# Kernel tuning notes

Measured on AMD Instinct MI355X. Metric: run time of the kernel, lower is better.

## Reference

```python
import jax, jax.numpy as jnp
import numpy as np

N_NODES = 50000
N_EDGES = 800000
IN_DIM = 6
HID = 256
OUT = 256
N_EXPERTS = 8
N_LAYERS = 2
N_GRAPHS = 64


def setup_inputs() -> dict:
    key = jax.random.key(0)
    ks = jax.random.split(key, 16)
    s = 0.05
    x = jax.random.normal(ks[0], (N_NODES, IN_DIM), dtype=jnp.float32)
    edge_index = jax.random.randint(ks[1], (2, N_EDGES), 0, N_NODES, dtype=jnp.int64)
    batch = jnp.sort(jax.random.randint(ks[2], (N_NODES,), 0, N_GRAPHS, dtype=jnp.int64))
    # shared encoder
    W_enc = jax.random.normal(ks[3], (IN_DIM, HID), jnp.float32) * s
    b_enc = jnp.zeros((HID,), jnp.float32)
    # router MLP: (HID+2) -> HID -> N_EXPERTS
    Wr1 = jax.random.normal(ks[4], (HID + 2, HID), jnp.float32) * s
    br1 = jnp.zeros((HID,), jnp.float32)
    Wr2 = jax.random.normal(ks[5], (HID, N_EXPERTS), jnp.float32) * s
    br2 = jnp.zeros((N_EXPERTS,), jnp.float32)
    # experts: 2 GraphConv layers each (self weight + neighbor weight + bias), stacked over experts
    Ws0 = jax.random.normal(ks[6], (N_EXPERTS, HID, HID), jnp.float32) * s
    Wn0 = jax.random.normal(ks[7], (N_EXPERTS, HID, HID), jnp.float32) * s
    b0 = jnp.zeros((N_EXPERTS, HID), jnp.float32)
    Ws1 = jax.random.normal(ks[8], (N_EXPERTS, HID, OUT), jnp.float32) * s
    Wn1 = jax.random.normal(ks[9], (N_EXPERTS, HID, OUT), jnp.float32) * s
    b1 = jnp.zeros((N_EXPERTS, OUT), jnp.float32)
    return dict(x=x, edge_index=edge_index, batch=batch, W_enc=W_enc, b_enc=b_enc,
                Wr1=Wr1, br1=br1, Wr2=Wr2, br2=br2,
                Ws0=Ws0, Wn0=Wn0, b0=b0, Ws1=Ws1, Wn1=Wn1, b1=b1)


def _graph_conv(h, src, dst, Ws, Wn, b):
    # PyG GraphConv: x' = x @ Ws + sum_{j in N(i)} x_j @ Wn + b
    msg = h[src] @ Wn                                   # [E, d_out]
    agg = jax.ops.segment_sum(msg, dst, num_segments=N_NODES)
    return h @ Ws + agg + b


def reference(x, edge_index, batch, W_enc, b_enc, Wr1, br1, Wr2, br2,
              Ws0, Wn0, b0, Ws1, Wn1, b1):
    src, dst = edge_index[0], edge_index[1]
    # shared encoder
    h = jax.nn.relu(x @ W_enc + b_enc)                  # [N, HID]
    # graph size features: per-graph node count and edge count, log-scaled, broadcast to nodes
    ones_n = jnp.ones((h.shape[0],), h.dtype)
    node_cnt = jax.ops.segment_sum(ones_n, batch, num_segments=N_GRAPHS)
    edge_cnt = jax.ops.segment_sum(jnp.ones((src.shape[0],), h.dtype), batch[src], num_segments=N_GRAPHS)
    size_feat = jnp.stack([jnp.log1p(node_cnt)[batch], jnp.log1p(edge_cnt)[batch]], axis=-1)  # [N, 2]
    # router -> top-1 expert index
    r = jax.nn.relu(jnp.concatenate([h, size_feat], axis=-1) @ Wr1 + br1)
    logits = r @ Wr2 + br2                              # [N, n_experts]
    idx = jnp.argmax(logits, axis=-1)                   # [N]
    # dense compute-all-experts, then gather by argmax (faithful to original)
    out = jnp.zeros((h.shape[0], Ws1.shape[-1]), h.dtype)
    for e in range(N_EXPERTS):
        z = jax.nn.relu(_graph_conv(h, src, dst, Ws0[e], Wn0[e], b0[e]))
        y_e = _graph_conv(z, src, dst, Ws1[e], Wn1[e], b1[e])   # [N, OUT]
        out = out + jnp.where((idx == e)[:, None], y_e, 0.0)
    return out
```

## Files before the change

kernel.cpp:

```cpp
#include <hip/hip_runtime.h>
#include <hip/hip_bf16.h>
#include <math.h>

#define NN 50000
#define NE 800000
#define NG 64
#define NEXP 8

#define BK 16
#define BM 64

typedef __attribute__((ext_vector_type(8))) short bf16x8;
typedef __attribute__((ext_vector_type(4))) float f32x4;
typedef unsigned short ushort_t;

__device__ __forceinline__ unsigned short f2bf(float f) {
  union { float f; unsigned u; } x; x.f = f;
  unsigned r = x.u + 0x7fff + ((x.u >> 16) & 1);
  return (unsigned short)(r >> 16);
}
__device__ __forceinline__ float bf2f(unsigned short u) {
  union { unsigned u; float f; } x; x.u = ((unsigned)u) << 16; return x.f;
}

__device__ __forceinline__ void gld16(const void* g, void* l) {
  __builtin_amdgcn_global_load_lds(
      (const __attribute__((address_space(1))) unsigned int*)g,
      (__attribute__((address_space(3))) unsigned int*)l, 16, 0, 0);
}

__global__ __launch_bounds__(256) void k_encoder(
    const float* __restrict__ x, const float* __restrict__ W,
    const float* __restrict__ b, float* __restrict__ H32,
    ushort_t* __restrict__ Xb, ushort_t* __restrict__ Xlo) {
  int i = blockIdx.x, n = threadIdx.x;
  float acc = b[n];
#pragma unroll
  for (int k = 0; k < 6; k++) acc = fmaf(x[i * 6 + k], W[k * 256 + n], acc);
  acc = fmaxf(acc, 0.f);
  H32[i * 256 + n] = acc;
  unsigned short hb = f2bf(acc);
  Xb[(size_t)i * 512 + n] = hb;
  Xlo[(size_t)i * 256 + n] = f2bf(acc - bf2f(hb));
}

__global__ __launch_bounds__(256) void k_count_nodes(
    const int* __restrict__ batch, int* __restrict__ node_cnt) {
  __shared__ int bins[NG];
  int t = threadIdx.x;
  if (t < NG) bins[t] = 0;
  __syncthreads();
  for (int i = blockIdx.x * blockDim.x + t; i < NN; i += gridDim.x * blockDim.x)
    atomicAdd(&bins[batch[i]], 1);
  __syncthreads();
  if (t < NG) atomicAdd(&node_cnt[t], bins[t]);
}

__global__ __launch_bounds__(256) void k_count_edges(
    const int* __restrict__ ei, const int* __restrict__ batch,
    int* __restrict__ edge_cnt, int* __restrict__ deg) {
  __shared__ int bins[NG];
  int t = threadIdx.x;
  if (t < NG) bins[t] = 0;
  __syncthreads();
  for (int e = blockIdx.x * blockDim.x + t; e < NE; e += gridDim.x * blockDim.x) {
    int s = ei[e];
    int d = ei[NE + e];
    atomicAdd(&bins[batch[s]], 1);
    atomicAdd(&deg[d], 1);
  }
  __syncthreads();
  if (t < NG) atomicAdd(&edge_cnt[t], bins[t]);
}

__global__ __launch_bounds__(256) void k_sizefeat(
    const int* __restrict__ batch, const int* __restrict__ node_cnt,
    const int* __restrict__ edge_cnt, float* __restrict__ sf0,
    float* __restrict__ sf1) {
  int i = blockIdx.x * blockDim.x + threadIdx.x;
  if (i < NN) {
    int g = batch[i];
    sf0[i] = log1pf((float)node_cnt[g]);
    sf1[i] = log1pf((float)edge_cnt[g]);
  }
}

__global__ __launch_bounds__(1024) void k_scan(
    const int* __restrict__ deg, int* __restrict__ offs, int* __restrict__ cursor) {
  __shared__ int wsums[16];
  int t = threadIdx.x, lane = t & 63, wid = t >> 6;
  int carry = 0;
  for (int base = 0; base < NN; base += 1024) {
    int i = base + t;
    int v = (i < NN) ? deg[i] : 0;
    int x = v;
#pragma unroll
    for (int d = 1; d < 64; d <<= 1) {
      int y = __shfl_up(x, d, 64);
      if (lane >= d) x += y;
    }
    if (lane == 63) wsums[wid] = x;
    __syncthreads();
    if (wid == 0) {
      int s = (lane < 16) ? wsums[lane] : 0;
#pragma unroll
      for (int d = 1; d < 16; d <<= 1) {
        int y = __shfl_up(s, d, 64);
        if (lane >= d) s += y;
      }
      if (lane < 16) wsums[lane] = s;
    }
    __syncthreads();
    int wpre = (wid > 0) ? wsums[wid - 1] : 0;
    int excl = carry + wpre + x - v;
    if (i < NN) { offs[i] = excl; cursor[i] = excl; }
    int btot = wsums[15];
    __syncthreads();
    carry += btot;
  }
  if (t == 0) offs[NN] = carry;
}

__global__ __launch_bounds__(256) void k_fill_csr(
    const int* __restrict__ ei, int* __restrict__ cursor, int* __restrict__ edge_src) {
  int e = blockIdx.x * blockDim.x + threadIdx.x;
  if (e < NE) {
    int d = ei[NE + e];
    int pos = atomicAdd(&cursor[d], 1);
    edge_src[pos] = ei[e];
  }
}

__global__ __launch_bounds__(256) void k_agg_h2(
    const int* __restrict__ offs, const int* __restrict__ edge_src,
    ushort_t* __restrict__ Xb) {
  int wid = threadIdx.x >> 6, lane = threadIdx.x & 63;
  int half = lane >> 5, cl = lane & 31;
  int i = blockIdx.x * 4 + wid;
  if (i >= NN) return;
  int e0 = offs[i], e1 = offs[i + 1];
  float acc[8] = {};
  int k = e0;
  for (; k + 4 <= e1; k += 4) {
    int s0 = edge_src[k + half];
    int s1 = edge_src[k + 2 + half];
    bf16x8 v0 = *(const bf16x8*)&Xb[(size_t)s0 * 512 + cl * 8];
    bf16x8 v1 = *(const bf16x8*)&Xb[(size_t)s1 * 512 + cl * 8];
#pragma unroll
    for (int j = 0; j < 8; j++) acc[j] += bf2f((unsigned short)v0[j]);
#pragma unroll
    for (int j = 0; j < 8; j++) acc[j] += bf2f((unsigned short)v1[j]);
  }
  for (; k + 2 <= e1; k += 2) {
    int s0 = edge_src[k + half];
    bf16x8 v0 = *(const bf16x8*)&Xb[(size_t)s0 * 512 + cl * 8];
#pragma unroll
    for (int j = 0; j < 8; j++) acc[j] += bf2f((unsigned short)v0[j]);
  }
  if (k < e1 && half == 0) {
    int s0 = edge_src[k];
    bf16x8 v0 = *(const bf16x8*)&Xb[(size_t)s0 * 512 + cl * 8];
#pragma unroll
    for (int j = 0; j < 8; j++) acc[j] += bf2f((unsigned short)v0[j]);
  }
#pragma unroll
  for (int j = 0; j < 8; j++) acc[j] += __shfl_xor(acc[j], 32, 64);
  if (half == 0) {
    bf16x8 o;
#pragma unroll
    for (int j = 0; j < 8; j++) o[j] = (short)f2bf(acc[j]);
    *(bf16x8*)(&Xb[(size_t)i * 512 + 256 + cl * 8]) = o;
  }
}

__global__ __launch_bounds__(256) void k_prep_w(
    const float* __restrict__ Ws0, const float* __restrict__ Wn0,
    const float* __restrict__ Ws1, const float* __restrict__ Wn1,
    ushort_t* __restrict__ Wt1, ushort_t* __restrict__ Wt2) {
  __shared__ float tile[32][33];
  int z = blockIdx.z;
  int e = z & 7;
  const float* Ws = (z < 8) ? Ws0 : Ws1;
  const float* Wn = (z < 8) ? Wn0 : Wn1;
  ushort_t* Wt = (z < 8) ? Wt1 : Wt2;
  int kt = blockIdx.x;
  int nt = blockIdx.y;
  int tx = threadIdx.x & 31, ty = threadIdx.x >> 5;
  const float* src = (kt < 8) ? (Ws + e * 65536 + (kt * 32) * 256)
                              : (Wn + e * 65536 + ((kt - 8) * 32) * 256);
#pragma unroll
  for (int rr = 0; rr < 32; rr += 8) {
    int k = rr + ty;
    tile[k][tx] = src[k * 256 + nt * 32 + tx];
  }
  __syncthreads();
#pragma unroll
  for (int rr = 0; rr < 32; rr += 8) {
    int n = rr + ty;
    Wt[(size_t)e * 131072 + (nt * 32 + n) * 512 + kt * 32 + tx] = f2bf(tile[tx][n]);
  }
}

__global__ __launch_bounds__(256) void k_prep_wr1(
    const float* __restrict__ Wr1, ushort_t* __restrict__ Wr1t) {
  int k = blockIdx.x;
  int n = threadIdx.x;
  unsigned short v;
  if (k < 256) {
    v = f2bf(Wr1[k * 256 + n]);
  } else if (k < 512) {
    float f = Wr1[(k - 256) * 256 + n];
    unsigned short h = f2bf(f);
    v = f2bf(f - bf2f(h));
  } else {
    v = f2bf(Wr1[(k - 512) * 256 + n]);
  }
  Wr1t[(size_t)n * 768 + k] = v;
}

__global__ __launch_bounds__(256) void k_router_mfma(
    const ushort_t* __restrict__ Xb,
    const ushort_t* __restrict__ Xlo,
    const ushort_t* __restrict__ Wr1t,
    const float* __restrict__ Wr1, const float* __restrict__ br1,
    const float* __restrict__ sf0, const float* __restrict__ sf1,
    float* __restrict__ R) {
  __shared__ ushort_t As[128 * 32];
  __shared__ ushort_t Bs[128 * 32];
  int t = threadIdx.x;
  int w = t >> 6, lane = t & 63;
  int m0 = blockIdx.x * 128;
  int n0 = blockIdx.y * 128;
  int wm = w >> 1, wn = w & 1;
  f32x4 acc[4][4] = {};
  for (int kt = 0; kt < 24; kt++) {
    int k0 = kt * 32;
    const ushort_t* Ab; int astr; int koff;
    if (kt < 8)       { Ab = Xb;  astr = 512; koff = k0; }
    else if (kt < 16) { Ab = Xb;  astr = 512; koff = k0 - 256; }
    else              { Ab = Xlo; astr = 256; koff = k0 - 512; }
#pragma unroll
    for (int i = 0; i < 2; i++) {
      int c = w * 128 + i * 64 + lane;
      int r = c >> 2, kc = c & 3;
      int gr = m0 + r; if (gr >= NN) gr = NN - 1;
      gld16(Ab + (size_t)gr * astr + koff + kc * 8,
            (void*)&As[(w * 128 + i * 64) * 8]);
      gld16(Wr1t + (size_t)(n0 + r) * 768 + k0 + kc * 8,
            (void*)&Bs[(w * 128 + i * 64) * 8]);
    }
    __syncthreads();
    bf16x8 a[4], b[4];
#pragma unroll
    for (int i = 0; i < 4; i++) {
      int ra = wm * 64 + i * 16 + (lane & 15);
      a[i] = *(const bf16x8*)&As[ra * 32 + (lane >> 4) * 8];
      int nb = wn * 64 + i * 16 + (lane & 15);
      b[i] = *(const bf16x8*)&Bs[nb * 32 + (lane >> 4) * 8];
    }
#pragma unroll
    for (int i = 0; i < 4; i++)
#pragma unroll
      for (int j = 0; j < 4; j++)
        acc[i][j] = __builtin_amdgcn_mfma_f32_16x16x32_bf16(a[i], b[j], acc[i][j], 0, 0, 0);
    __syncthreads();
  }
  int q = lane >> 4, c15 = lane & 15;
#pragma unroll
  for (int i = 0; i < 4; i++) {
#pragma unroll
    for (int j = 0; j < 4; j++) {
      int col = n0 + wn * 64 + j * 16 + c15;
      float bias = br1[col];
      float w6 = Wr1[65536 + col];
      float w7 = Wr1[65792 + col];
#pragma unroll
      for (int v = 0; v < 4; v++) {
        int lrow = wm * 64 + i * 16 + q * 4 + v;
        int row = m0 + lrow;
        if (row < NN)
          R[(size_t)row * 256 + col] =
              fmaxf(acc[i][j][v] + bias + sf0[row] * w6 + sf1[row] * w7, 0.f);
      }
    }
  }
}

#define TIE_TAU 1e-4f
__global__ __launch_bounds__(256) void k_logits(
    const float* __restrict__ R, const float* __restrict__ Wr2,
    const float* __restrict__ br2, int* __restrict__ idx,
    int* __restrict__ nfix, int* __restrict__ fixlist) {
  int t = threadIdx.x, wid = t >> 6, lane = t & 63;
  int i = blockIdx.x * 4 + wid;
  if (i < NN) {
    float4 r4 = *(const float4*)(&R[i * 256 + lane * 4]);
    float rv[4] = {r4.x, r4.y, r4.z, r4.w};
    float acc[NEXP] = {};
#pragma unroll
    for (int kk = 0; kk < 4; kk++) {
      int k = lane * 4 + kk;
#pragma unroll
      for (int e = 0; e < NEXP; e++) acc[e] = fmaf(rv[kk], Wr2[k * 8 + e], acc[e]);
    }
#pragma unroll
    for (int d = 32; d > 0; d >>= 1)
#pragma unroll
      for (int e = 0; e < NEXP; e++) acc[e] += __shfl_xor(acc[e], d, 64);
    if (lane == 0) {
      float best = -1e30f, second = -1e30f; int bi = 0;
      for (int e = 0; e < NEXP; e++) {
        float v = acc[e] + br2[e];
        if (v > best) { second = best; best = v; bi = e; }
        else if (v > second) second = v;
      }
      idx[i] = bi;
      if (best - second < TIE_TAU) {
        int p = atomicAdd(nfix, 1);
        fixlist[p] = i;
      }
    }
  }
}

__global__ __launch_bounds__(256) void k_fixup(
    const float* __restrict__ H32, const float* __restrict__ Wr1,
    const float* __restrict__ br1, const float* __restrict__ Wr2,
    const float* __restrict__ br2, const float* __restrict__ sf0,
    const float* __restrict__ sf1, const int* __restrict__ fixlist,
    const int* __restrict__ nfix, int* __restrict__ idx) {
  __shared__ float lred[4][NEXP];
  int n = *nfix;
  int t = threadIdx.x, wid = t >> 6, lane = t & 63;
  for (int q = blockIdx.x; q < n; q += gridDim.x) {
    int node = fixlist[q];
    float acc = br1[t] + sf0[node] * Wr1[65536 + t] + sf1[node] * Wr1[65792 + t];
    for (int k = 0; k < 256; k++)
      acc = fmaf(H32[(size_t)node * 256 + k], Wr1[k * 256 + t], acc);
    float r = fmaxf(acc, 0.f);
    float le[NEXP];
#pragma unroll
    for (int e = 0; e < NEXP; e++) le[e] = r * Wr2[t * 8 + e];
#pragma unroll
    for (int d = 32; d > 0; d >>= 1)
#pragma unroll
      for (int e = 0; e < NEXP; e++) le[e] += __shfl_xor(le[e], d, 64);
    if (lane == 0) {
#pragma unroll
      for (int e = 0; e < NEXP; e++) lred[wid][e] = le[e];
    }
    __syncthreads();
    if (t == 0) {
      float best = -1e30f; int bi = 0;
      for (int e = 0; e < NEXP; e++) {
        float v = lred[0][e] + lred[1][e] + lred[2][e] + lred[3][e] + br2[e];
        if (v > best) { best = v; bi = e; }
      }
      idx[node] = bi;
    }
    __syncthreads();
  }
}

__global__ __launch_bounds__(256) void k_ecnt(
    const int* __restrict__ idx, int* __restrict__ ecnt) {
  __shared__ int bins[NEXP];
  int t = threadIdx.x;
  if (t < NEXP) bins[t] = 0;
  __syncthreads();
  for (int i = blockIdx.x * 256 + t; i < NN; i += gridDim.x * 256)
    atomicAdd(&bins[idx[i]], 1);
  __syncthreads();
  if (t < NEXP) atomicAdd(&ecnt[t], bins[t]);
}

__global__ __launch_bounds__(256) void k_srcmask(
    const int* __restrict__ ei, const int* __restrict__ idx,
    unsigned int* __restrict__ mask) {
  int k = blockIdx.x * 256 + threadIdx.x;
  if (k < NE) {
    int s = ei[k], d = ei[NE + k];
    atomicOr(&mask[s], 1u << idx[d]);
  }
  if (k < NN) atomicOr(&mask[k], 1u << idx[k]);
}

__global__ __launch_bounds__(256) void k_scount(
    const unsigned int* __restrict__ mask, int* __restrict__ scnt) {
  __shared__ int bins[NEXP];
  int t = threadIdx.x;
  if (t < NEXP) bins[t] = 0;
  __syncthreads();
  for (int i = blockIdx.x * 256 + t; i < NN; i += gridDim.x * 256) {
    unsigned m = mask[i];
    while (m) { int b = __ffs(m) - 1; atomicAdd(&bins[b], 1); m &= m - 1; }
  }
  __syncthreads();
  if (t < NEXP) atomicAdd(&scnt[t], bins[t]);
}

__global__ void k_bucket_offs(const int* __restrict__ ecnt,
                              const int* __restrict__ scnt,
                              int* __restrict__ boff, int* __restrict__ bcur,
                              int* __restrict__ tstart,
                              int* __restrict__ soff, int* __restrict__ scur) {
  if (threadIdx.x == 0) {
    int s = 0, ts = 0, s2 = 0;
    for (int e = 0; e < NEXP; e++) {
      boff[e] = s; bcur[e] = s;
      tstart[e] = ts;
      ts += (ecnt[e] + 127) / 128;
      s += ecnt[e];
      soff[e] = s2; scur[e] = s2;
      s2 += scnt[e];
    }
    boff[NEXP] = s;
    tstart[NEXP] = ts;
    soff[NEXP] = s2;
  }
}

#define BF_BLOCKS 64
__global__ __launch_bounds__(256) void k_bucket_fill2(
    const int* __restrict__ idx, int* __restrict__ bcur, int* __restrict__ nlist) {
  __shared__ int lcnt[NEXP];
  __shared__ int lbase[NEXP];
  int t = threadIdx.x;
  int chunk = (NN + BF_BLOCKS - 1) / BF_BLOCKS;
  int lo = blockIdx.x * chunk;
  int hi = lo + chunk; if (hi > NN) hi = NN;
  if (t < NEXP) lcnt[t] = 0;
  __syncthreads();
  for (int i = lo + t; i < hi; i += 256) atomicAdd(&lcnt[idx[i]], 1);
  __syncthreads();
  if (t < NEXP) lbase[t] = atomicAdd(&bcur[t], lcnt[t]);
  __syncthreads();
  if (t < NEXP) lcnt[t] = 0;
  __syncthreads();
  for (int i = lo + t; i < hi; i += 256) {
    int e = idx[i];
    int p = atomicAdd(&lcnt[e], 1);
    nlist[lbase[e] + p] = i;
  }
}

__global__ __launch_bounds__(256) void k_scompact(
    const unsigned int* __restrict__ mask, int* __restrict__ scur,
    int* __restrict__ slist) {
  __shared__ int lcnt[NEXP];
  __shared__ int lbase[NEXP];
  int t = threadIdx.x;
  int chunk = (NN + BF_BLOCKS - 1) / BF_BLOCKS;
  int lo = blockIdx.x * chunk;
  int hi = lo + chunk; if (hi > NN) hi = NN;
  if (t < NEXP) lcnt[t] = 0;
  __syncthreads();
  for (int i = lo + t; i < hi; i += 256) {
    unsigned m = mask[i];
    while (m) { int b = __ffs(m) - 1; atomicAdd(&lcnt[b], 1); m &= m - 1; }
  }
  __syncthreads();
  if (t < NEXP) lbase[t] = atomicAdd(&scur[t], lcnt[t]);
  __syncthreads();
  if (t < NEXP) lcnt[t] = 0;
  __syncthreads();
  for (int i = lo + t; i < hi; i += 256) {
    unsigned m = mask[i];
    while (m) {
      int b = __ffs(m) - 1;
      int p = atomicAdd(&lcnt[b], 1);
      slist[lbase[b] + p] = i;
      m &= m - 1;
    }
  }
}

__global__ __launch_bounds__(256) void k_layer1_rows(
    const ushort_t* __restrict__ Abf,
    const ushort_t* __restrict__ Wt,
    const float* __restrict__ b0, const int* __restrict__ idx,
    const int* __restrict__ slist, const int* __restrict__ soff, int e,
    ushort_t* __restrict__ Zb, ushort_t* __restrict__ A2) {
  int base = soff[e];
  int cnt = soff[e + 1] - base;
  int m0 = blockIdx.x * 128;
  if (m0 >= cnt) return;
  __shared__ ushort_t As[128 * 32];
  __shared__ ushort_t Bs[128 * 32];
  __shared__ int rows[128];
  __shared__ int sidx[128];
  int t = threadIdx.x;
  if (t < 128) {
    int r = (m0 + t < cnt) ? slist[base + m0 + t] : -1;
    rows[t] = r;
    sidx[t] = (r >= 0) ? idx[r] : -1;
  }
  __syncthreads();
  int w = t >> 6, lane = t & 63;
  int n0 = blockIdx.y * 128;
  int wm = w >> 1, wn = w & 1;
  const ushort_t* Wb = Wt + (size_t)e * 131072;

  f32x4 acc[4][4] = {};

  for (int kt = 0; kt < 16; kt++) {
    int k0 = kt * 32;
#pragma unroll
    for (int i = 0; i < 2; i++) {
      int c = w * 128 + i * 64 + lane;
      int r = c >> 2, kc = c & 3;
      int nd = rows[r]; if (nd < 0) nd = 0;
      gld16(Abf + (size_t)nd * 512 + k0 + kc * 8,
            (void*)&As[(w * 128 + i * 64) * 8]);
      gld16(Wb + (size_t)(n0 + r) * 512 + k0 + kc * 8,
            (void*)&Bs[(w * 128 + i * 64) * 8]);
    }
    __syncthreads();
    bf16x8 a[4], b[4];
#pragma unroll
    for (int i = 0; i < 4; i++) {
      int ra = wm * 64 + i * 16 + (lane & 15);
      a[i] = *(const bf16x8*)&As[ra * 32 + (lane >> 4) * 8];
      int nb = wn * 64 + i * 16 + (lane & 15);
      b[i] = *(const bf16x8*)&Bs[nb * 32 + (lane >> 4) * 8];
    }
#pragma unroll
    for (int i = 0; i < 4; i++)
#pragma unroll
      for (int j = 0; j < 4; j++)
        acc[i][j] = __builtin_amdgcn_mfma_f32_16x16x32_bf16(a[i], b[j], acc[i][j], 0, 0, 0);
    __syncthreads();
  }
  int q = lane >> 4, c15 = lane & 15;
#pragma unroll
  for (int i = 0; i < 4; i++) {
#pragma unroll
    for (int j = 0; j < 4; j++) {
      int col = n0 + wn * 64 + j * 16 + c15;
      float bias = b0[e * 256 + col];
#pragma unroll
      for (int v = 0; v < 4; v++) {
        int lrow = wm * 64 + i * 16 + q * 4 + v;
        int node = rows[lrow];
        if (node >= 0) {
          unsigned short zb = f2bf(fmaxf(acc[i][j][v] + bias, 0.f));
          Zb[(size_t)node * 256 + col] = zb;
          if (sidx[lrow] == e) A2[(size_t)node * 512 + col] = zb;
        }
      }
    }
  }
}

__global__ __launch_bounds__(256) void k_agg_z2(
    const ushort_t* __restrict__ Zb, const int* __restrict__ offs,
    const int* __restrict__ edge_src, const int* __restrict__ nlist,
    const int* __restrict__ boff, int e, ushort_t* __restrict__ A2) {
  int wid = threadIdx.x >> 6, lane = threadIdx.x & 63;
  int half = lane >> 5, cl = lane & 31;
  int b = blockIdx.x * 4 + wid;
  int base = boff[e];
  int cnt = boff[e + 1] - base;
  if (b >= cnt) return;
  int i = nlist[base + b];
  int e0 = offs[i], e1 = offs[i + 1];
  float acc[8] = {};
  int k = e0;
  for (; k + 4 <= e1; k += 4) {
    int s0 = edge_src[k + half];
    int s1 = edge_src[k + 2 + half];
    bf16x8 v0 = *(const bf16x8*)&Zb[(size_t)s0 * 256 + cl * 8];
    bf16x8 v1 = *(const bf16x8*)&Zb[(size_t)s1 * 256 + cl * 8];
#pragma unroll
    for (int j = 0; j < 8; j++) acc[j] += bf2f((unsigned short)v0[j]);
#pragma unroll
    for (int j = 0; j < 8; j++) acc[j] += bf2f((unsigned short)v1[j]);
  }
  for (; k + 2 <= e1; k += 2) {
    int s0 = edge_src[k + half];
    bf16x8 v0 = *(const bf16x8*)&Zb[(size_t)s0 * 256 + cl * 8];
#pragma unroll
    for (int j = 0; j < 8; j++) acc[j] += bf2f((unsigned short)v0[j]);
  }
  if (k < e1 && half == 0) {
    int s0 = edge_src[k];
    bf16x8 v0 = *(const bf16x8*)&Zb[(size_t)s0 * 256 + cl * 8];
#pragma unroll
    for (int j = 0; j < 8; j++) acc[j] += bf2f((unsigned short)v0[j]);
  }
#pragma unroll
  for (int j = 0; j < 8; j++) acc[j] += __shfl_xor(acc[j], 32, 64);
  if (half == 0) {
    bf16x8 o;
#pragma unroll
    for (int j = 0; j < 8; j++) o[j] = (short)f2bf(acc[j]);
    *(bf16x8*)(&A2[(size_t)i * 512 + 256 + cl * 8]) = o;
  }
}

#define MAXT2 (391 + NEXP)
__global__ __launch_bounds__(256) void k_layer2_mfma(
    const ushort_t* __restrict__ A2,
    const ushort_t* __restrict__ Wt,
    const float* __restrict__ b1, const int* __restrict__ nlist,
    const int* __restrict__ boff, const int* __restrict__ tstart,
    float* __restrict__ outp) {
  __shared__ ushort_t As[128 * 32];
  __shared__ ushort_t Bs[128 * 32];
  __shared__ int rows[128];
  int t = threadIdx.x;
  int tx = blockIdx.x;
  int e = -1;
#pragma unroll
  for (int q = 0; q < NEXP; q++)
    if (tx >= tstart[q] && tx < tstart[q + 1]) e = q;
  if (e < 0) return;
  int tile = tx - tstart[e];
  int base = boff[e];
  int cnt = boff[e + 1] - base;
  int m0 = tile * 128;
  if (t < 128) rows[t] = (m0 + t < cnt) ? nlist[base + m0 + t] : -1;
  __syncthreads();
  int w = t >> 6, lane = t & 63;
  int n0 = blockIdx.y * 128;
  int wm = w >> 1, wn = w & 1;
  const ushort_t* Wb = Wt + (size_t)e * 131072;

  f32x4 acc[4][4] = {};

  for (int kt = 0; kt < 16; kt++) {
    int k0 = kt * 32;
#pragma unroll
    for (int i = 0; i < 2; i++) {
      int c = w * 128 + i * 64 + lane;
      int r = c >> 2, kc = c & 3;
      int nd = rows[r]; if (nd < 0) nd = 0;
      gld16(A2 + (size_t)nd * 512 + k0 + kc * 8,
            (void*)&As[(w * 128 + i * 64) * 8]);
      gld16(Wb + (size_t)(n0 + r) * 512 + k0 + kc * 8,
            (void*)&Bs[(w * 128 + i * 64) * 8]);
    }
    __syncthreads();
    bf16x8 a[4], b[4];
#pragma unroll
    for (int i = 0; i < 4; i++) {
      int ra = wm * 64 + i * 16 + (lane & 15);
      a[i] = *(const bf16x8*)&As[ra * 32 + (lane >> 4) * 8];
      int nb = wn * 64 + i * 16 + (lane & 15);
      b[i] = *(const bf16x8*)&Bs[nb * 32 + (lane >> 4) * 8];
    }
#pragma unroll
    for (int i = 0; i < 4; i++)
#pragma unroll
      for (int j = 0; j < 4; j++)
        acc[i][j] = __builtin_amdgcn_mfma_f32_16x16x32_bf16(a[i], b[j], acc[i][j], 0, 0, 0);
    __syncthreads();
  }
  int q = lane >> 4, c15 = lane & 15;
#pragma unroll
  for (int i = 0; i < 4; i++) {
#pragma unroll
    for (int j = 0; j < 4; j++) {
      int col = n0 + wn * 64 + j * 16 + c15;
      float bias = b1[e * 256 + col];
#pragma unroll
      for (int v = 0; v < 4; v++) {
        int lrow = wm * 64 + i * 16 + q * 4 + v;
        int node = rows[lrow];
        if (node >= 0) outp[(size_t)node * 256 + col] = acc[i][j][v] + bias;
      }
    }
  }
}

static inline char* wsalloc(char*& p, size_t bytes) {
  char* r = p;
  p += (bytes + 255) & ~(size_t)255;
  return r;
}

extern "C" void kernel_launch(void* const* d_in, const int* in_sizes, int n_in,
                              void* d_out, int out_size, void* d_ws, size_t ws_size,
                              hipStream_t stream) {
  const float* x     = (const float*)d_in[0];
  const int*   ei    = (const int*)d_in[1];
  const int*   batch = (const int*)d_in[2];
  const float* W_enc = (const float*)d_in[3];
  const float* b_enc = (const float*)d_in[4];
  const float* Wr1   = (const float*)d_in[5];
  const float* br1   = (const float*)d_in[6];
  const float* Wr2   = (const float*)d_in[7];
  const float* br2   = (const float*)d_in[8];
  const float* Ws0   = (const float*)d_in[9];
  const float* Wn0   = (const float*)d_in[10];
  const float* b0    = (const float*)d_in[11];
  const float* Ws1   = (const float*)d_in[12];
  const float* Wn1   = (const float*)d_in[13];
  const float* b1    = (const float*)d_in[14];
  float* outp = (float*)d_out;

  char* p = (char*)d_ws;
  float*    H32  = (float*)wsalloc(p, (size_t)NN * 256 * 4);
  ushort_t* Xb   = (ushort_t*)wsalloc(p, (size_t)NN * 512 * 2);
  ushort_t* Zb   = (ushort_t*)wsalloc(p, (size_t)NN * 256 * 2);
  ushort_t* A2   = (ushort_t*)wsalloc(p, (size_t)NN * 512 * 2);
  float*    R    = (float*)A2;
  ushort_t* Xlo  = Zb;
  ushort_t* Wt1  = (ushort_t*)wsalloc(p, (size_t)NEXP * 256 * 512 * 2);
  ushort_t* Wt2  = (ushort_t*)wsalloc(p, (size_t)NEXP * 256 * 512 * 2);
  ushort_t* Wr1t = (ushort_t*)wsalloc(p, (size_t)256 * 768 * 2);
  int* edge_src  = (int*)wsalloc(p, (size_t)NE * 4);
  int* offs      = (int*)wsalloc(p, (size_t)(NN + 1) * 4);
  int* cursor    = (int*)wsalloc(p, (size_t)NN * 4);
  int* deg       = (int*)wsalloc(p, (size_t)NN * 4);
  int* idxb      = (int*)wsalloc(p, (size_t)NN * 4);
  float* sf0     = (float*)wsalloc(p, (size_t)NN * 4);
  float* sf1     = (float*)wsalloc(p, (size_t)NN * 4);
  int* nlist     = (int*)wsalloc(p, (size_t)NN * 4);
  int* fixlist   = (int*)wsalloc(p, (size_t)NN * 4);
  unsigned int* maskb = (unsigned int*)wsalloc(p, (size_t)NN * 4);
  int* slist     = (int*)wsalloc(p, (size_t)NN * NEXP * 4);
  int* smallb    = (int*)wsalloc(p, 256 * 4);
  int* node_cnt = smallb;
  int* edge_cnt = smallb + 64;
  int* ecnt     = smallb + 128;
  int* boff     = smallb + 136;
  int* bcur     = smallb + 152;
  int* tstart   = smallb + 160;
  int* nfix     = smallb + 192;
  int* scnt     = smallb + 200;
  int* soff     = smallb + 208;
  int* scur     = smallb + 224;

  hipMemsetAsync(deg, 0, (size_t)NN * 4, stream);
  hipMemsetAsync(smallb, 0, 256 * 4, stream);
  hipMemsetAsync(maskb, 0, (size_t)NN * 4, stream);

  k_encoder<<<NN, 256, 0, stream>>>(x, W_enc, b_enc, H32, Xb, Xlo);
  k_count_nodes<<<64, 256, 0, stream>>>(batch, node_cnt);
  k_count_edges<<<128, 256, 0, stream>>>(ei, batch, edge_cnt, deg);
  k_sizefeat<<<(NN + 255) / 256, 256, 0, stream>>>(batch, node_cnt, edge_cnt, sf0, sf1);
  k_scan<<<1, 1024, 0, stream>>>(deg, offs, cursor);
  k_fill_csr<<<(NE + 255) / 256, 256, 0, stream>>>(ei, cursor, edge_src);
  k_agg_h2<<<(NN + 3) / 4, 256, 0, stream>>>(offs, edge_src, Xb);
  k_prep_w<<<dim3(16, 8, 16), 256, 0, stream>>>(Ws0, Wn0, Ws1, Wn1, Wt1, Wt2);
  k_prep_wr1<<<768, 256, 0, stream>>>(Wr1, Wr1t);
  k_router_mfma<<<dim3((NN + 127) / 128, 2), 256, 0, stream>>>(
      Xb, Xlo, Wr1t, Wr1, br1, sf0, sf1, R);
  k_logits<<<(NN + 3) / 4, 256, 0, stream>>>(R, Wr2, br2, idxb, nfix, fixlist);
  k_fixup<<<256, 256, 0, stream>>>(H32, Wr1, br1, Wr2, br2, sf0, sf1,
                                   fixlist, nfix, idxb);
  k_srcmask<<<(NE + 255) / 256, 256, 0, stream>>>(ei, idxb, maskb);
  k_ecnt<<<64, 256, 0, stream>>>(idxb, ecnt);
  k_scount<<<64, 256, 0, stream>>>(maskb, scnt);
  k_bucket_offs<<<1, 64, 0, stream>>>(ecnt, scnt, boff, bcur, tstart, soff, scur);
  k_bucket_fill2<<<BF_BLOCKS, 256, 0, stream>>>(idxb, bcur, nlist);
  k_scompact<<<BF_BLOCKS, 256, 0, stream>>>(maskb, scur, slist);
  for (int e = 0; e < NEXP; e++) {
    k_layer1_rows<<<dim3((NN + 127) / 128, 2), 256, 0, stream>>>(
        Xb, Wt1, b0, idxb, slist, soff, e, Zb, A2);
    k_agg_z2<<<(NN + 3) / 4, 256, 0, stream>>>(Zb, offs, edge_src, nlist, boff, e, A2);
  }
  k_layer2_mfma<<<dim3(MAXT2, 2), 256, 0, stream>>>(
      A2, Wt2, b1, nlist, boff, tstart, outp);
}
```

Baseline: 699.9 us.

## Fuse router logits into MFMA GEMM, double-buffer GEMMs, drop H32, widen gathers

```diff
diff --git a/kernel.cpp b/kernel.cpp
--- a/kernel.cpp
+++ b/kernel.cpp
@@ -7,9 +7,6 @@
 #define NG 64
 #define NEXP 8
 
-#define BK 16
-#define BM 64
-
 typedef __attribute__((ext_vector_type(8))) short bf16x8;
 typedef __attribute__((ext_vector_type(4))) float f32x4;
 typedef unsigned short ushort_t;
@@ -31,14 +28,13 @@
 
 __global__ __launch_bounds__(256) void k_encoder(
     const float* __restrict__ x, const float* __restrict__ W,
-    const float* __restrict__ b, float* __restrict__ H32,
-    ushort_t* __restrict__ Xb, ushort_t* __restrict__ Xlo) {
+    const float* __restrict__ b, ushort_t* __restrict__ Xb,
+    ushort_t* __restrict__ Xlo) {
   int i = blockIdx.x, n = threadIdx.x;
   float acc = b[n];
 #pragma unroll
   for (int k = 0; k < 6; k++) acc = fmaf(x[i * 6 + k], W[k * 256 + n], acc);
   acc = fmaxf(acc, 0.f);
-  H32[i * 256 + n] = acc;
   unsigned short hb = f2bf(acc);
   Xb[(size_t)i * 512 + n] = hb;
   Xlo[(size_t)i * 256 + n] = f2bf(acc - bf2f(hb));
@@ -141,15 +137,23 @@
   int e0 = offs[i], e1 = offs[i + 1];
   float acc[8] = {};
   int k = e0;
-  for (; k + 4 <= e1; k += 4) {
+  for (; k + 8 <= e1; k += 8) {
     int s0 = edge_src[k + half];
     int s1 = edge_src[k + 2 + half];
+    int s2 = edge_src[k + 4 + half];
+    int s3 = edge_src[k + 6 + half];
     bf16x8 v0 = *(const bf16x8*)&Xb[(size_t)s0 * 512 + cl * 8];
     bf16x8 v1 = *(const bf16x8*)&Xb[(size_t)s1 * 512 + cl * 8];
+    bf16x8 v2 = *(const bf16x8*)&Xb[(size_t)s2 * 512 + cl * 8];
+    bf16x8 v3 = *(const bf16x8*)&Xb[(size_t)s3 * 512 + cl * 8];
 #pragma unroll
     for (int j = 0; j < 8; j++) acc[j] += bf2f((unsigned short)v0[j]);
 #pragma unroll
     for (int j = 0; j < 8; j++) acc[j] += bf2f((unsigned short)v1[j]);
+#pragma unroll
+    for (int j = 0; j < 8; j++) acc[j] += bf2f((unsigned short)v2[j]);
+#pragma unroll
+    for (int j = 0; j < 8; j++) acc[j] += bf2f((unsigned short)v3[j]);
   }
   for (; k + 2 <= e1; k += 2) {
     int s0 = edge_src[k + half];
@@ -208,135 +212,191 @@
   unsigned short v;
   if (k < 256) {
     v = f2bf(Wr1[k * 256 + n]);
-  } else if (k < 512) {
+  } else {
     float f = Wr1[(k - 256) * 256 + n];
     unsigned short h = f2bf(f);
     v = f2bf(f - bf2f(h));
-  } else {
-    v = f2bf(Wr1[(k - 512) * 256 + n]);
-  }
-  Wr1t[(size_t)n * 768 + k] = v;
-}
-
+  }
+  Wr1t[(size_t)n * 512 + k] = v;
+}
+
+#define TIE_TAU 1e-4f
 __global__ __launch_bounds__(256) void k_router_mfma(
     const ushort_t* __restrict__ Xb,
     const ushort_t* __restrict__ Xlo,
     const ushort_t* __restrict__ Wr1t,
     const float* __restrict__ Wr1, const float* __restrict__ br1,
-    const float* __restrict__ sf0, const float* __restrict__ sf1,
-    float* __restrict__ R) {
-  __shared__ ushort_t As[128 * 32];
-  __shared__ ushort_t Bs[128 * 32];
+    const float* __restrict__ Wr2, const float* __restrict__ sf0,
+    const float* __restrict__ sf1, float* __restrict__ Lpart) {
+  __shared__ ushort_t As[2][4096];
+  __shared__ ushort_t Bs1[2][4096];
+  __shared__ ushort_t Bs2[2][4096];
+  __shared__ float Lsm[128][NEXP];
   int t = threadIdx.x;
   int w = t >> 6, lane = t & 63;
   int m0 = blockIdx.x * 128;
   int n0 = blockIdx.y * 128;
   int wm = w >> 1, wn = w & 1;
-  f32x4 acc[4][4] = {};
-  for (int kt = 0; kt < 24; kt++) {
-    int k0 = kt * 32;
-    const ushort_t* Ab; int astr; int koff;
-    if (kt < 8)       { Ab = Xb;  astr = 512; koff = k0; }
-    else if (kt < 16) { Ab = Xb;  astr = 512; koff = k0 - 256; }
-    else              { Ab = Xlo; astr = 256; koff = k0 - 512; }
+  for (int z = t; z < 128 * NEXP; z += 256) ((float*)Lsm)[z] = 0.f;
+
+  auto STAGE = [&](int s, int kt) {
+    int k0 = (kt & 7) * 32;
+    bool hi = kt < 8;
 #pragma unroll
     for (int i = 0; i < 2; i++) {
       int c = w * 128 + i * 64 + lane;
       int r = c >> 2, kc = c & 3;
       int gr = m0 + r; if (gr >= NN) gr = NN - 1;
-      gld16(Ab + (size_t)gr * astr + koff + kc * 8,
-            (void*)&As[(w * 128 + i * 64) * 8]);
-      gld16(Wr1t + (size_t)(n0 + r) * 768 + k0 + kc * 8,
-            (void*)&Bs[(w * 128 + i * 64) * 8]);
-    }
-    __syncthreads();
-    bf16x8 a[4], b[4];
+      int dst = (w * 128 + i * 64) * 8;
+      if (hi) {
+        gld16(Xb + (size_t)gr * 512 + k0 + kc * 8, (void*)&As[s][dst]);
+        gld16(Wr1t + (size_t)(n0 + r) * 512 + k0 + kc * 8, (void*)&Bs1[s][dst]);
+        gld16(Wr1t + (size_t)(n0 + r) * 512 + 256 + k0 + kc * 8, (void*)&Bs2[s][dst]);
+      } else {
+        gld16(Xlo + (size_t)gr * 256 + k0 + kc * 8, (void*)&As[s][dst]);
+        gld16(Wr1t + (size_t)(n0 + r) * 512 + k0 + kc * 8, (void*)&Bs1[s][dst]);
+      }
+    }
+  };
+
+  f32x4 acc[4][4] = {};
+  STAGE(0, 0);
+  __syncthreads();
+  for (int kt = 0; kt < 16; kt++) {
+    int cur = kt & 1;
+    if (kt < 15) STAGE(cur ^ 1, kt + 1);
+    bf16x8 a[4], b1[4];
 #pragma unroll
     for (int i = 0; i < 4; i++) {
       int ra = wm * 64 + i * 16 + (lane & 15);
-      a[i] = *(const bf16x8*)&As[ra * 32 + (lane >> 4) * 8];
+      a[i] = *(const bf16x8*)&As[cur][ra * 32 + (lane >> 4) * 8];
       int nb = wn * 64 + i * 16 + (lane & 15);
-      b[i] = *(const bf16x8*)&Bs[nb * 32 + (lane >> 4) * 8];
+      b1[i] = *(const bf16x8*)&Bs1[cur][nb * 32 + (lane >> 4) * 8];
     }
 #pragma unroll
     for (int i = 0; i < 4; i++)
 #pragma unroll
       for (int j = 0; j < 4; j++)
-        acc[i][j] = __builtin_amdgcn_mfma_f32_16x16x32_bf16(a[i], b[j], acc[i][j], 0, 0, 0);
+        acc[i][j] = __builtin_amdgcn_mfma_f32_16x16x32_bf16(a[i], b1[j], acc[i][j], 0, 0, 0);
+    if (kt < 8) {
+      bf16x8 b2[4];
+#pragma unroll
+      for (int i = 0; i < 4; i++) {
+        int nb = wn * 64 + i * 16 + (lane & 15);
+        b2[i] = *(const bf16x8*)&Bs2[cur][nb * 32 + (lane >> 4) * 8];
+      }
+#pragma unroll
+      for (int i = 0; i < 4; i++)
+#pragma unroll
+        for (int j = 0; j < 4; j++)
+          acc[i][j] = __builtin_amdgcn_mfma_f32_16x16x32_bf16(a[i], b2[j], acc[i][j], 0, 0, 0);
+    }
     __syncthreads();
   }
+
   int q = lane >> 4, c15 = lane & 15;
-#pragma unroll
-  for (int i = 0; i < 4; i++) {
-#pragma unroll
-    for (int j = 0; j < 4; j++) {
-      int col = n0 + wn * 64 + j * 16 + c15;
-      float bias = br1[col];
-      float w6 = Wr1[65536 + col];
-      float w7 = Wr1[65792 + col];
+  float bb[4], w6[4], w7[4];
+#pragma unroll
+  for (int j = 0; j < 4; j++) {
+    int col = n0 + wn * 64 + j * 16 + c15;
+    bb[j] = br1[col];
+    w6[j] = Wr1[65536 + col];
+    w7[j] = Wr1[65792 + col];
+  }
+#pragma unroll
+  for (int i = 0; i < 4; i++)
+#pragma unroll
+    for (int v = 0; v < 4; v++) {
+      int row = m0 + wm * 64 + i * 16 + q * 4 + v;
+      float s0v = (row < NN) ? sf0[row] : 0.f;
+      float s1v = (row < NN) ? sf1[row] : 0.f;
+#pragma unroll
+      for (int j = 0; j < 4; j++)
+        acc[i][j][v] = fmaxf(acc[i][j][v] + bb[j] + s0v * w6[j] + s1v * w7[j], 0.f);
+    }
+#pragma unroll
+  for (int e = 0; e < NEXP; e++) {
+    float wr2j[4];
+#pragma unroll
+    for (int j = 0; j < 4; j++)
+      wr2j[j] = Wr2[(n0 + wn * 64 + j * 16 + c15) * 8 + e];
+    float pe[4][4];
+#pragma unroll
+    for (int i = 0; i < 4; i++)
 #pragma unroll
       for (int v = 0; v < 4; v++) {
-        int lrow = wm * 64 + i * 16 + q * 4 + v;
-        int row = m0 + lrow;
-        if (row < NN)
-          R[(size_t)row * 256 + col] =
-              fmaxf(acc[i][j][v] + bias + sf0[row] * w6 + sf1[row] * w7, 0.f);
+        float s = acc[i][0][v] * wr2j[0];
+        s = fmaf(acc[i][1][v], wr2j[1], s);
+        s = fmaf(acc[i][2][v], wr2j[2], s);
+        s = fmaf(acc[i][3][v], wr2j[3], s);
+        pe[i][v] = s;
       }
-    }
-  }
-}
-
-#define TIE_TAU 1e-4f
-__global__ __launch_bounds__(256) void k_logits(
-    const float* __restrict__ R, const float* __restrict__ Wr2,
-    const float* __restrict__ br2, int* __restrict__ idx,
-    int* __restrict__ nfix, int* __restrict__ fixlist) {
-  int t = threadIdx.x, wid = t >> 6, lane = t & 63;
-  int i = blockIdx.x * 4 + wid;
-  if (i < NN) {
-    float4 r4 = *(const float4*)(&R[i * 256 + lane * 4]);
-    float rv[4] = {r4.x, r4.y, r4.z, r4.w};
-    float acc[NEXP] = {};
-#pragma unroll
-    for (int kk = 0; kk < 4; kk++) {
-      int k = lane * 4 + kk;
-#pragma unroll
-      for (int e = 0; e < NEXP; e++) acc[e] = fmaf(rv[kk], Wr2[k * 8 + e], acc[e]);
-    }
-#pragma unroll
-    for (int d = 32; d > 0; d >>= 1)
-#pragma unroll
-      for (int e = 0; e < NEXP; e++) acc[e] += __shfl_xor(acc[e], d, 64);
-    if (lane == 0) {
-      float best = -1e30f, second = -1e30f; int bi = 0;
-      for (int e = 0; e < NEXP; e++) {
-        float v = acc[e] + br2[e];
-        if (v > best) { second = best; best = v; bi = e; }
-        else if (v > second) second = v;
-      }
-      idx[i] = bi;
-      if (best - second < TIE_TAU) {
-        int p = atomicAdd(nfix, 1);
-        fixlist[p] = i;
-      }
-    }
+#pragma unroll
+    for (int d = 1; d < 16; d <<= 1)
+#pragma unroll
+      for (int i = 0; i < 4; i++)
+#pragma unroll
+        for (int v = 0; v < 4; v++)
+          pe[i][v] += __shfl_xor(pe[i][v], d, 64);
+    if (c15 == 0) {
+#pragma unroll
+      for (int i = 0; i < 4; i++)
+#pragma unroll
+        for (int v = 0; v < 4; v++)
+          atomicAdd(&Lsm[wm * 64 + i * 16 + q * 4 + v][e], pe[i][v]);
+    }
+  }
+  __syncthreads();
+  for (int z = t; z < 128 * NEXP; z += 256) {
+    int lr = z >> 3, e = z & 7;
+    int row = m0 + lr;
+    if (row < NN)
+      Lpart[(size_t)blockIdx.y * NN * 8 + (size_t)row * 8 + e] = Lsm[lr][e];
+  }
+}
+
+__global__ __launch_bounds__(256) void k_argmax(
+    const float* __restrict__ Lpart, const float* __restrict__ br2,
+    int* __restrict__ idx, int* __restrict__ nfix, int* __restrict__ fixlist) {
+  int i = blockIdx.x * 256 + threadIdx.x;
+  if (i >= NN) return;
+  float best = -1e30f, second = -1e30f; int bi = 0;
+#pragma unroll
+  for (int e = 0; e < NEXP; e++) {
+    float v = Lpart[(size_t)i * 8 + e] + Lpart[(size_t)NN * 8 + (size_t)i * 8 + e]
+              + br2[e];
+    if (v > best) { second = best; best = v; bi = e; }
+    else if (v > second) second = v;
+  }
+  idx[i] = bi;
+  if (best - second < TIE_TAU) {
+    int p = atomicAdd(nfix, 1);
+    fixlist[p] = i;
   }
 }
 
 __global__ __launch_bounds__(256) void k_fixup(
-    const float* __restrict__ H32, const float* __restrict__ Wr1,
+    const float* __restrict__ x, const float* __restrict__ W_enc,
+    const float* __restrict__ b_enc, const float* __restrict__ Wr1,
     const float* __restrict__ br1, const float* __restrict__ Wr2,
     const float* __restrict__ br2, const float* __restrict__ sf0,
     const float* __restrict__ sf1, const int* __restrict__ fixlist,
     const int* __restrict__ nfix, int* __restrict__ idx) {
+  __shared__ float hsh[256];
   __shared__ float lred[4][NEXP];
   int n = *nfix;
   int t = threadIdx.x, wid = t >> 6, lane = t & 63;
-  for (int q = blockIdx.x; q < n; q += gridDim.x) {
-    int node = fixlist[q];
+  for (int qq = blockIdx.x; qq < n; qq += gridDim.x) {
+    int node = fixlist[qq];
+    float hv = b_enc[t];
+#pragma unroll
+    for (int k = 0; k < 6; k++)
+      hv = fmaf(x[node * 6 + k], W_enc[k * 256 + t], hv);
+    hsh[t] = fmaxf(hv, 0.f);
+    __syncthreads();
     float acc = br1[t] + sf0[node] * Wr1[65536 + t] + sf1[node] * Wr1[65792 + t];
     for (int k = 0; k < 256; k++)
-      acc = fmaf(H32[(size_t)node * 256 + k], Wr1[k * 256 + t], acc);
+      acc = fmaf(hsh[k], Wr1[k * 256 + t], acc);
     float r = fmaxf(acc, 0.f);
     float le[NEXP];
 #pragma unroll
@@ -485,8 +545,8 @@
   int cnt = soff[e + 1] - base;
   int m0 = blockIdx.x * 128;
   if (m0 >= cnt) return;
-  __shared__ ushort_t As[128 * 32];
-  __shared__ ushort_t Bs[128 * 32];
+  __shared__ ushort_t As[2][4096];
+  __shared__ ushort_t Bs[2][4096];
   __shared__ int rows[128];
   __shared__ int sidx[128];
   int t = threadIdx.x;
@@ -501,28 +561,32 @@
   int wm = w >> 1, wn = w & 1;
   const ushort_t* Wb = Wt + (size_t)e * 131072;
 
-  f32x4 acc[4][4] = {};
-
-  for (int kt = 0; kt < 16; kt++) {
+  auto STAGE = [&](int s, int kt) {
     int k0 = kt * 32;
 #pragma unroll
     for (int i = 0; i < 2; i++) {
       int c = w * 128 + i * 64 + lane;
       int r = c >> 2, kc = c & 3;
       int nd = rows[r]; if (nd < 0) nd = 0;
-      gld16(Abf + (size_t)nd * 512 + k0 + kc * 8,
-            (void*)&As[(w * 128 + i * 64) * 8]);
-      gld16(Wb + (size_t)(n0 + r) * 512 + k0 + kc * 8,
-            (void*)&Bs[(w * 128 + i * 64) * 8]);
-    }
-    __syncthreads();
+      int dst = (w * 128 + i * 64) * 8;
+      gld16(Abf + (size_t)nd * 512 + k0 + kc * 8, (void*)&As[s][dst]);
+      gld16(Wb + (size_t)(n0 + r) * 512 + k0 + kc * 8, (void*)&Bs[s][dst]);
+    }
+  };
+
+  f32x4 acc[4][4] = {};
+  STAGE(0, 0);
+  __syncthreads();
+  for (int kt = 0; kt < 16; kt++) {
+    int cur = kt & 1;
+    if (kt < 15) STAGE(cur ^ 1, kt + 1);
     bf16x8 a[4], b[4];
 #pragma unroll
     for (int i = 0; i < 4; i++) {
       int ra = wm * 64 + i * 16 + (lane & 15);
-      a[i] = *(const bf16x8*)&As[ra * 32 + (lane >> 4) * 8];
+      a[i] = *(const bf16x8*)&As[cur][ra * 32 + (lane >> 4) * 8];
       int nb = wn * 64 + i * 16 + (lane & 15);
-      b[i] = *(const bf16x8*)&Bs[nb * 32 + (lane >> 4) * 8];
+      b[i] = *(const bf16x8*)&Bs[cur][nb * 32 + (lane >> 4) * 8];
     }
 #pragma unroll
     for (int i = 0; i < 4; i++)
@@ -558,43 +622,51 @@
     const int* __restrict__ boff, int e, ushort_t* __restrict__ A2) {
   int wid = threadIdx.x >> 6, lane = threadIdx.x & 63;
   int half = lane >> 5, cl = lane & 31;
-  int b = blockIdx.x * 4 + wid;
   int base = boff[e];
   int cnt = boff[e + 1] - base;
-  if (b >= cnt) return;
-  int i = nlist[base + b];
-  int e0 = offs[i], e1 = offs[i + 1];
-  float acc[8] = {};
-  int k = e0;
-  for (; k + 4 <= e1; k += 4) {
-    int s0 = edge_src[k + half];
-    int s1 = edge_src[k + 2 + half];
-    bf16x8 v0 = *(const bf16x8*)&Zb[(size_t)s0 * 256 + cl * 8];
-    bf16x8 v1 = *(const bf16x8*)&Zb[(size_t)s1 * 256 + cl * 8];
-#pragma unroll
-    for (int j = 0; j < 8; j++) acc[j] += bf2f((unsigned short)v0[j]);
-#pragma unroll
-    for (int j = 0; j < 8; j++) acc[j] += bf2f((unsigned short)v1[j]);
-  }
-  for (; k + 2 <= e1; k += 2) {
-    int s0 = edge_src[k + half];
-    bf16x8 v0 = *(const bf16x8*)&Zb[(size_t)s0 * 256 + cl * 8];
-#pragma unroll
-    for (int j = 0; j < 8; j++) acc[j] += bf2f((unsigned short)v0[j]);
-  }
-  if (k < e1 && half == 0) {
-    int s0 = edge_src[k];
-    bf16x8 v0 = *(const bf16x8*)&Zb[(size_t)s0 * 256 + cl * 8];
-#pragma unroll
-    for (int j = 0; j < 8; j++) acc[j] += bf2f((unsigned short)v0[j]);
-  }
-#pragma unroll
-  for (int j = 0; j < 8; j++) acc[j] += __shfl_xor(acc[j], 32, 64);
-  if (half == 0) {
-    bf16x8 o;
-#pragma unroll
-    for (int j = 0; j < 8; j++) o[j] = (short)f2bf(acc[j]);
-    *(bf16x8*)(&A2[(size_t)i * 512 + 256 + cl * 8]) = o;
+  for (int b = blockIdx.x * 4 + wid; b < cnt; b += gridDim.x * 4) {
+    int i = nlist[base + b];
+    int e0 = offs[i], e1 = offs[i + 1];
+    float acc[8] = {};
+    int k = e0;
+    for (; k + 8 <= e1; k += 8) {
+      int s0 = edge_src[k + half];
+      int s1 = edge_src[k + 2 + half];
+      int s2 = edge_src[k + 4 + half];
+      int s3 = edge_src[k + 6 + half];
+      bf16x8 v0 = *(const bf16x8*)&Zb[(size_t)s0 * 256 + cl * 8];
+      bf16x8 v1 = *(const bf16x8*)&Zb[(size_t)s1 * 256 + cl * 8];
+      bf16x8 v2 = *(const bf16x8*)&Zb[(size_t)s2 * 256 + cl * 8];
+      bf16x8 v3 = *(const bf16x8*)&Zb[(size_t)s3 * 256 + cl * 8];
+#pragma unroll
+      for (int j = 0; j < 8; j++) acc[j] += bf2f((unsigned short)v0[j]);
+#pragma unroll
+      for (int j = 0; j < 8; j++) acc[j] += bf2f((unsigned short)v1[j]);
+#pragma unroll
+      for (int j = 0; j < 8; j++) acc[j] += bf2f((unsigned short)v2[j]);
+#pragma unroll
+      for (int j = 0; j < 8; j++) acc[j] += bf2f((unsigned short)v3[j]);
+    }
+    for (; k + 2 <= e1; k += 2) {
+      int s0 = edge_src[k + half];
+      bf16x8 v0 = *(const bf16x8*)&Zb[(size_t)s0 * 256 + cl * 8];
+#pragma unroll
+      for (int j = 0; j < 8; j++) acc[j] += bf2f((unsigned short)v0[j]);
+    }
+    if (k < e1 && half == 0) {
+      int s0 = edge_src[k];
+      bf16x8 v0 = *(const bf16x8*)&Zb[(size_t)s0 * 256 + cl * 8];
+#pragma unroll
+      for (int j = 0; j < 8; j++) acc[j] += bf2f((unsigned short)v0[j]);
+    }
+#pragma unroll
+    for (int j = 0; j < 8; j++) acc[j] += __shfl_xor(acc[j], 32, 64);
+    if (half == 0) {
+      bf16x8 o;
+#pragma unroll
+      for (int j = 0; j < 8; j++) o[j] = (short)f2bf(acc[j]);
+      *(bf16x8*)(&A2[(size_t)i * 512 + 256 + cl * 8]) = o;
+    }
   }
 }
 
@@ -605,8 +677,8 @@
     const float* __restrict__ b1, const int* __restrict__ nlist,
     const int* __restrict__ boff, const int* __restrict__ tstart,
     float* __restrict__ outp) {
-  __shared__ ushort_t As[128 * 32];
-  __shared__ ushort_t Bs[128 * 32];
+  __shared__ ushort_t As[2][4096];
+  __shared__ ushort_t Bs[2][4096];
   __shared__ int rows[128];
   int t = threadIdx.x;
   int tx = blockIdx.x;
@@ -626,28 +698,32 @@
   int wm = w >> 1, wn = w & 1;
   const ushort_t* Wb = Wt + (size_t)e * 131072;
 
-  f32x4 acc[4][4] = {};
-
-  for (int kt = 0; kt < 16; kt++) {
+  auto STAGE = [&](int s, int kt) {
     int k0 = kt * 32;
 #pragma unroll
     for (int i = 0; i < 2; i++) {
       int c = w * 128 + i * 64 + lane;
       int r = c >> 2, kc = c & 3;
       int nd = rows[r]; if (nd < 0) nd = 0;
-      gld16(A2 + (size_t)nd * 512 + k0 + kc * 8,
-            (void*)&As[(w * 128 + i * 64) * 8]);
-      gld16(Wb + (size_t)(n0 + r) * 512 + k0 + kc * 8,
-            (void*)&Bs[(w * 128 + i * 64) * 8]);
-    }
-    __syncthreads();
+      int dst = (w * 128 + i * 64) * 8;
+      gld16(A2 + (size_t)nd * 512 + k0 + kc * 8, (void*)&As[s][dst]);
+      gld16(Wb + (size_t)(n0 + r) * 512 + k0 + kc * 8, (void*)&Bs[s][dst]);
+    }
+  };
+
+  f32x4 acc[4][4] = {};
+  STAGE(0, 0);
+  __syncthreads();
+  for (int kt = 0; kt < 16; kt++) {
+    int cur = kt & 1;
+    if (kt < 15) STAGE(cur ^ 1, kt + 1);
     bf16x8 a[4], b[4];
 #pragma unroll
     for (int i = 0; i < 4; i++) {
       int ra = wm * 64 + i * 16 + (lane & 15);
-      a[i] = *(const bf16x8*)&As[ra * 32 + (lane >> 4) * 8];
+      a[i] = *(const bf16x8*)&As[cur][ra * 32 + (lane >> 4) * 8];
       int nb = wn * 64 + i * 16 + (lane & 15);
-      b[i] = *(const bf16x8*)&Bs[nb * 32 + (lane >> 4) * 8];
+      b[i] = *(const bf16x8*)&Bs[cur][nb * 32 + (lane >> 4) * 8];
     }
 #pragma unroll
     for (int i = 0; i < 4; i++)
@@ -700,15 +776,14 @@
   float* outp = (float*)d_out;
 
   char* p = (char*)d_ws;
-  float*    H32  = (float*)wsalloc(p, (size_t)NN * 256 * 4);
   ushort_t* Xb   = (ushort_t*)wsalloc(p, (size_t)NN * 512 * 2);
   ushort_t* Zb   = (ushort_t*)wsalloc(p, (size_t)NN * 256 * 2);
   ushort_t* A2   = (ushort_t*)wsalloc(p, (size_t)NN * 512 * 2);
-  float*    R    = (float*)A2;
   ushort_t* Xlo  = Zb;
+  float*    Lpart= (float*)wsalloc(p, (size_t)2 * NN * 8 * 4);
   ushort_t* Wt1  = (ushort_t*)wsalloc(p, (size_t)NEXP * 256 * 512 * 2);
   ushort_t* Wt2  = (ushort_t*)wsalloc(p, (size_t)NEXP * 256 * 512 * 2);
-  ushort_t* Wr1t = (ushort_t*)wsalloc(p, (size_t)256 * 768 * 2);
+  ushort_t* Wr1t = (ushort_t*)wsalloc(p, (size_t)256 * 512 * 2);
   int* edge_src  = (int*)wsalloc(p, (size_t)NE * 4);
   int* offs      = (int*)wsalloc(p, (size_t)(NN + 1) * 4);
   int* cursor    = (int*)wsalloc(p, (size_t)NN * 4);
@@ -736,7 +811,7 @@
   hipMemsetAsync(smallb, 0, 256 * 4, stream);
   hipMemsetAsync(maskb, 0, (size_t)NN * 4, stream);
 
-  k_encoder<<<NN, 256, 0, stream>>>(x, W_enc, b_enc, H32, Xb, Xlo);
+  k_encoder<<<NN, 256, 0, stream>>>(x, W_enc, b_enc, Xb, Xlo);
   k_count_nodes<<<64, 256, 0, stream>>>(batch, node_cnt);
   k_count_edges<<<128, 256, 0, stream>>>(ei, batch, edge_cnt, deg);
   k_sizefeat<<<(NN + 255) / 256, 256, 0, stream>>>(batch, node_cnt, edge_cnt, sf0, sf1);
@@ -744,12 +819,12 @@
   k_fill_csr<<<(NE + 255) / 256, 256, 0, stream>>>(ei, cursor, edge_src);
   k_agg_h2<<<(NN + 3) / 4, 256, 0, stream>>>(offs, edge_src, Xb);
   k_prep_w<<<dim3(16, 8, 16), 256, 0, stream>>>(Ws0, Wn0, Ws1, Wn1, Wt1, Wt2);
-  k_prep_wr1<<<768, 256, 0, stream>>>(Wr1, Wr1t);
+  k_prep_wr1<<<512, 256, 0, stream>>>(Wr1, Wr1t);
   k_router_mfma<<<dim3((NN + 127) / 128, 2), 256, 0, stream>>>(
-      Xb, Xlo, Wr1t, Wr1, br1, sf0, sf1, R);
-  k_logits<<<(NN + 3) / 4, 256, 0, stream>>>(R, Wr2, br2, idxb, nfix, fixlist);
-  k_fixup<<<256, 256, 0, stream>>>(H32, Wr1, br1, Wr2, br2, sf0, sf1,
-                                   fixlist, nfix, idxb);
+      Xb, Xlo, Wr1t, Wr1, br1, Wr2, sf0, sf1, Lpart);
+  k_argmax<<<(NN + 255) / 256, 256, 0, stream>>>(Lpart, br2, idxb, nfix, fixlist);
+  k_fixup<<<256, 256, 0, stream>>>(x, W_enc, b_enc, Wr1, br1, Wr2, br2,
+                                   sf0, sf1, fixlist, nfix, idxb);
   k_srcmask<<<(NE + 255) / 256, 256, 0, stream>>>(ei, idxb, maskb);
   k_ecnt<<<64, 256, 0, stream>>>(idxb, ecnt);
   k_scount<<<64, 256, 0, stream>>>(maskb, scnt);
@@ -759,7 +834,7 @@
   for (int e = 0; e < NEXP; e++) {
     k_layer1_rows<<<dim3((NN + 127) / 128, 2), 256, 0, stream>>>(
         Xb, Wt1, b0, idxb, slist, soff, e, Zb, A2);
-    k_agg_z2<<<(NN + 3) / 4, 256, 0, stream>>>(Zb, offs, edge_src, nlist, boff, e, A2);
+    k_agg_z2<<<3125, 256, 0, stream>>>(Zb, offs, edge_src, nlist, boff, e, A2);
   }
   k_layer2_mfma<<<dim3(MAXT2, 2), 256, 0, stream>>>(
       A2, Wt2, b1, nlist, boff, tstart, outp);
```

Measured after the change: 645.5 us. -7.8%, faster.
